# Optimization experiments

Measured on AMD Instinct MI355X. Metric: run time of the kernel, lower is better.

Reference implementation:

```python
import jax, jax.numpy as jnp
import numpy as np

# ---- module config (matches __init__ defaults) ----
NUM_EL_FULL = 128
LV_START, LV_END = 31, 95
NUM_S = LV_END - LV_START            # 64 sensors
NX = NY = 408
ROI = 128
DX = DY = 0.0002
C0 = 1500.0
FS = 40.0e6
DT = 1.0 / FS
R_IN = 0.0406
ARC_ANGLE = 270.0
ARC_START = 135.0
T_SAMPLES = 2030
BATCH = 64


def _geometry():
    """Reproduce _precompute_geometry + _precompute_time_indices_and_weights in numpy."""
    spacing = ARC_ANGLE / (NUM_EL_FULL - 1)
    all_ang = ARC_START + np.arange(NUM_EL_FULL) * spacing
    ang = all_ang[LV_START:LV_END]
    ang_rad = ang * np.pi / 180.0
    cx = (NX / 2 - 0.5) * DX
    cy = (NY / 2 - 0.5) * DY
    sx = cx + R_IN * np.cos(ang_rad)
    sy = cy + R_IN * np.sin(ang_rad)

    rsx = round((NX - ROI) / 2)
    rsy = round((NY - ROI) / 2)
    x_pos = (np.arange(rsx, rsx + ROI, dtype=np.float32) * DX)
    y_pos = (np.arange(rsy, rsy + ROI, dtype=np.float32) * DY)
    yg, xg = np.meshgrid(y_pos, x_pos, indexing='ij')  # [ROI, ROI]

    x_diff = xg[..., None] - sx[None, None, :]          # [ROI, ROI, S]
    y_diff = yg[..., None] - sy[None, None, :]
    dist = np.sqrt(x_diff ** 2 + y_diff ** 2)
    t_idx = np.round(dist / C0 / DT).astype(np.int32)

    normal = ang_rad + np.pi
    a2p = np.arctan2(y_diff, x_diff)
    adiff = a2p - normal[None, None, :]
    adiff = np.arctan2(np.sin(adiff), np.cos(adiff))
    weights = np.clip(np.cos(adiff), 0.0, None).astype(np.float32)
    valid = (t_idx >= 0) & (t_idx < T_SAMPLES)
    return t_idx, weights, valid


def setup_inputs() -> dict:
    key = jax.random.key(0)
    t_idx, weights, valid = _geometry()
    sinogram = jax.random.normal(key, (BATCH, 1, NUM_S, T_SAMPLES), dtype=jnp.float32)
    return {
        "sinogram": sinogram,
        "weights": jnp.asarray(weights),
        "time_indices": jnp.asarray(t_idx),
        "valid_mask": jnp.asarray(valid),
    }


def reference(sinogram, weights, time_indices, valid_mask):
    """DAS beamforming, output_type='both', norm_type='clamp'."""
    B = sinogram.shape[0]
    T = sinogram.shape[-1]
    sino = sinogram[:, 0]                                   # [B, S, T]
    S = sino.shape[1]
    t = jnp.clip(time_indices, 0, T - 1)                    # [H, W, S]
    sensor_idx = jnp.arange(S)[None, None, :]               # [1, 1, S]
    # gather: per-pixel, per-sensor time sample -> [B, H, W, S]
    sampled = sino[:, sensor_idx, t]
    w = jnp.where(valid_mask, weights, 0.0)                 # mask * weight fused
    weighted = sampled * w[None]                            # [B, H, W, S]

    das = weighted.sum(axis=3)[:, None]                     # [B, 1, H, W]
    # normalize: clamp to >=0, per-batch max
    das = jnp.maximum(das, 0.0)
    m = das.reshape(B, -1).max(axis=1)
    m = jnp.where(m > 1e-8, m, 1.0)
    das = das / m[:, None, None, None]

    pixel_interp = jnp.transpose(weighted, (0, 3, 1, 2))    # [B, S, H, W]
    return das, pixel_interp
```

## Files before the change

### kernel.cpp

```cpp
#include <hip/hip_runtime.h>
#include <stdint.h>

#define NB   64
#define NS   64
#define NT   2030
#define NP   16384
#define DAS_ELEMS (NB * NP)
#define PIX_ELEMS ((size_t)NB * NS * NP)

typedef float v4f __attribute__((ext_vector_type(4)));

__global__ __launch_bounds__(256) void prep_kernel(
    const int* __restrict__ t_idx, const float* __restrict__ w,
    int* __restrict__ tc, float* __restrict__ wv)
{
    __shared__ int   ti[64][65];
    __shared__ float wf[64][65];
    const int pbase = blockIdx.x * 64;

    #pragma unroll
    for (int k = 0; k < 16; ++k) {
        int o = k * 256 + threadIdx.x;
        int r = o >> 6, s = o & 63;
        ti[r][s] = t_idx[pbase * 64 + o];
        wf[r][s] = w[pbase * 64 + o];
    }
    __syncthreads();

    #pragma unroll
    for (int k = 0; k < 16; ++k) {
        int o = k * 256 + threadIdx.x;
        int s = o >> 6, r = o & 63;
        int t = ti[r][s];
        bool valid = (t >= 0) & (t < NT);
        int tcl = min(max(t, 0), NT - 1);
        tc[s * NP + pbase + r] = tcl;
        wv[s * NP + pbase + r] = valid ? wf[r][s] : 0.0f;
    }
}

__global__ __launch_bounds__(256) void main_lds_kernel(
    const float* __restrict__ sino,
    const int*   __restrict__ tptr,
    const float* __restrict__ wptr,
    float*       __restrict__ das,
    float*       __restrict__ pix,
    unsigned*    __restrict__ bmax)
{
    __shared__ float lds[2][2048];

    const int tid = threadIdx.x;
    const int b = blockIdx.y;
    const int p = blockIdx.x * 1024 + tid * 4;
    const float* __restrict__ srow = sino + (size_t)b * (NS * NT);
    float* __restrict__ pixb = pix + (size_t)b * ((size_t)NS * NP) + p;

    {
        const float2* __restrict__ r = (const float2*)srow;
        float2 a0 = r[tid];
        float2 a1 = r[tid + 256];
        float2 a2 = r[tid + 512];
        float2* D = (float2*)lds[0];
        D[tid]       = a0;
        D[tid + 256] = a1;
        D[tid + 512] = a2;
        if (tid < 247) D[tid + 768] = r[tid + 768];
    }
    __syncthreads();

    v4f acc = (v4f)(0.0f);
    int cur = 0;

    for (int s = 0; s < NS; ++s) {
        float2 a0, a1, a2, a3;
        if (s + 1 < NS) {
            const float2* __restrict__ r = (const float2*)(srow + (s + 1) * NT);
            a0 = r[tid];
            a1 = r[tid + 256];
            a2 = r[tid + 512];
            if (tid < 247) a3 = r[tid + 768];
        }

        const float* __restrict__ L = lds[cur];
        const int4   t  = *(const int4*)  (tptr + s * NP + p);
        const float4 w4 = *(const float4*)(wptr + s * NP + p);
        v4f v;
        v.x = L[t.x] * w4.x;
        v.y = L[t.y] * w4.y;
        v.z = L[t.z] * w4.z;
        v.w = L[t.w] * w4.w;
        __builtin_nontemporal_store(v, (v4f*)(pixb + (size_t)s * NP));
        acc += v;

        if (s + 1 < NS) {
            float2* D = (float2*)lds[cur ^ 1];
            D[tid]       = a0;
            D[tid + 256] = a1;
            D[tid + 512] = a2;
            if (tid < 247) D[tid + 768] = a3;
            cur ^= 1;
        }
        __syncthreads();
    }

    acc.x = fmaxf(acc.x, 0.f); acc.y = fmaxf(acc.y, 0.f);
    acc.z = fmaxf(acc.z, 0.f); acc.w = fmaxf(acc.w, 0.f);
    *(v4f*)(das + (size_t)b * NP + p) = acc;

    float m = fmaxf(fmaxf(acc.x, acc.y), fmaxf(acc.z, acc.w));
    #pragma unroll
    for (int off = 32; off > 0; off >>= 1)
        m = fmaxf(m, __shfl_down(m, off, 64));
    __shared__ float wm[4];
    if ((tid & 63) == 0) wm[tid >> 6] = m;
    __syncthreads();
    if (tid == 0) {
        m = fmaxf(fmaxf(wm[0], wm[1]), fmaxf(wm[2], wm[3]));
        atomicMax(&bmax[b], __float_as_uint(m));
    }
}

__global__ __launch_bounds__(256) void main_fallback_kernel(
    const float* __restrict__ sino,
    const int*   __restrict__ tptr,
    const float* __restrict__ wptr,
    float*       __restrict__ das,
    float*       __restrict__ pix,
    unsigned*    __restrict__ bmax)
{
    const int b = blockIdx.y;
    const int p = blockIdx.x * 1024 + threadIdx.x * 4;
    const float* __restrict__ srow = sino + (size_t)b * (NS * NT);
    float* __restrict__ pixb = pix + (size_t)b * ((size_t)NS * NP) + p;

    v4f acc = (v4f)(0.0f);

    for (int s = 0; s < NS; ++s) {
        int t0 = tptr[(p + 0) * NS + s];
        int t1 = tptr[(p + 1) * NS + s];
        int t2 = tptr[(p + 2) * NS + s];
        int t3 = tptr[(p + 3) * NS + s];
        float wx = ((t0 >= 0) & (t0 < NT)) ? wptr[(p + 0) * NS + s] : 0.f;
        float wy = ((t1 >= 0) & (t1 < NT)) ? wptr[(p + 1) * NS + s] : 0.f;
        float wz = ((t2 >= 0) & (t2 < NT)) ? wptr[(p + 2) * NS + s] : 0.f;
        float ww = ((t3 >= 0) & (t3 < NT)) ? wptr[(p + 3) * NS + s] : 0.f;
        int4 t;
        t.x = min(max(t0, 0), NT - 1);
        t.y = min(max(t1, 0), NT - 1);
        t.z = min(max(t2, 0), NT - 1);
        t.w = min(max(t3, 0), NT - 1);
        const float* __restrict__ sr = srow + s * NT;
        v4f v;
        v.x = sr[t.x] * wx;
        v.y = sr[t.y] * wy;
        v.z = sr[t.z] * wz;
        v.w = sr[t.w] * ww;
        __builtin_nontemporal_store(v, (v4f*)(pixb + (size_t)s * NP));
        acc += v;
    }

    acc.x = fmaxf(acc.x, 0.f); acc.y = fmaxf(acc.y, 0.f);
    acc.z = fmaxf(acc.z, 0.f); acc.w = fmaxf(acc.w, 0.f);
    *(v4f*)(das + (size_t)b * NP + p) = acc;

    float m = fmaxf(fmaxf(acc.x, acc.y), fmaxf(acc.z, acc.w));
    #pragma unroll
    for (int off = 32; off > 0; off >>= 1)
        m = fmaxf(m, __shfl_down(m, off, 64));
    __shared__ float wm[4];
    if ((threadIdx.x & 63) == 0) wm[threadIdx.x >> 6] = m;
    __syncthreads();
    if (threadIdx.x == 0) {
        m = fmaxf(fmaxf(wm[0], wm[1]), fmaxf(wm[2], wm[3]));
        atomicMax(&bmax[b], __float_as_uint(m));
    }
}

__global__ __launch_bounds__(256) void norm_kernel(
    float* __restrict__ das, const unsigned* __restrict__ bmax)
{
    int idx = (blockIdx.x * 256 + threadIdx.x) * 4;
    int b = idx >> 14;
    float m = __uint_as_float(bmax[b]);
    m = (m > 1e-8f) ? m : 1.0f;
    v4f v = *(v4f*)(das + idx);
    v.x = v.x / m; v.y = v.y / m; v.z = v.z / m; v.w = v.w / m;
    *(v4f*)(das + idx) = v;
}

extern "C" void kernel_launch(void* const* d_in, const int* in_sizes, int n_in,
                              void* d_out, int out_size, void* d_ws, size_t ws_size,
                              hipStream_t stream)
{
    const float* sino  = (const float*)d_in[0];
    const float* w     = (const float*)d_in[1];
    const int*   t_idx = (const int*)  d_in[2];

    float* das = (float*)d_out;
    float* pix = (float*)d_out + DAS_ELEMS;

    char* ws = (char*)d_ws;
    const size_t need = (size_t)(8u << 20) + 256;
    const bool big = ws_size >= need;

    unsigned* bmax;
    int* tc = nullptr; float* wv = nullptr;
    if (big) {
        tc   = (int*)ws;
        wv   = (float*)(ws + (4u << 20));
        bmax = (unsigned*)(ws + (8u << 20));
    } else {
        bmax = (unsigned*)ws;
    }

    (void)hipMemsetAsync(bmax, 0, NB * sizeof(unsigned), stream);

    if (big) {
        prep_kernel<<<256, 256, 0, stream>>>(t_idx, w, tc, wv);
        main_lds_kernel<<<dim3(16, NB), 256, 0, stream>>>(sino, tc, wv, das, pix, bmax);
    } else {
        main_fallback_kernel<<<dim3(16, NB), 256, 0, stream>>>(sino, t_idx, w, das, pix, bmax);
    }
    norm_kernel<<<DAS_ELEMS / 1024, 256, 0, stream>>>(das, bmax);
}
```

Measured before the change: 392.8 us.

## Stage per-wavefront sinogram windows in LDS and drop block barriers

Each wavefront now computes the minimum time index over its pixels for each sensor and copies a private 1024-sample window of that sensor's row into its own double-buffered LDS slice. This removes the block-wide __syncthreads per sensor iteration. Time indices and weights are also prefetched two sensors ahead in registers. The cost is redundant global reads across the four waves. Correctness also depends on each wave's index span fitting inside the window, which holds for this fixed array geometry but is not checked.

```diff
diff --git a/kernel.cpp b/kernel.cpp
--- a/kernel.cpp
+++ b/kernel.cpp
@@ -7,6 +7,8 @@
 #define NP   16384
 #define DAS_ELEMS (NB * NP)
 #define PIX_ELEMS ((size_t)NB * NS * NP)
+
+#define WIN 1024
 
 typedef float v4f __attribute__((ext_vector_type(4)));
 
@@ -47,60 +49,82 @@
     float*       __restrict__ pix,
     unsigned*    __restrict__ bmax)
 {
-    __shared__ float lds[2][2048];
-
-    const int tid = threadIdx.x;
+    __shared__ float sbuf[4][2][WIN];
+
+    const int tid  = threadIdx.x;
+    const int wid  = tid >> 6;
+    const int lane = tid & 63;
     const int b = blockIdx.y;
     const int p = blockIdx.x * 1024 + tid * 4;
     const float* __restrict__ srow = sino + (size_t)b * (NS * NT);
     float* __restrict__ pixb = pix + (size_t)b * ((size_t)NS * NP) + p;
-
+    float* const Lb = &sbuf[wid][0][0];
+
+    int4   tq_cur = *(const int4*)  (tptr + 0 * NP + p);
+    float4 wq_cur = *(const float4*)(wptr + 0 * NP + p);
+    int4   tq_n1  = *(const int4*)  (tptr + 1 * NP + p);
+    float4 wq_n1  = *(const float4*)(wptr + 1 * NP + p);
+
+    int m0 = min(min(tq_cur.x, tq_cur.y), min(tq_cur.z, tq_cur.w));
+    #pragma unroll
+    for (int off = 32; off > 0; off >>= 1)
+        m0 = min(m0, __shfl_xor(m0, off, 64));
+    int w0c = min(m0, NT - WIN) & ~1;
     {
-        const float2* __restrict__ r = (const float2*)srow;
-        float2 a0 = r[tid];
-        float2 a1 = r[tid + 256];
-        float2 a2 = r[tid + 512];
-        float2* D = (float2*)lds[0];
-        D[tid]       = a0;
-        D[tid + 256] = a1;
-        D[tid + 512] = a2;
-        if (tid < 247) D[tid + 768] = r[tid + 768];
-    }
-    __syncthreads();
+        const float2* __restrict__ rr = (const float2*)(srow + w0c);
+        float2* __restrict__ D = (float2*)Lb;
+        #pragma unroll
+        for (int k = 0; k < 8; ++k)
+            D[lane + 64 * k] = rr[lane + 64 * k];
+    }
+    int cur = 0;
 
     v4f acc = (v4f)(0.0f);
-    int cur = 0;
 
     for (int s = 0; s < NS; ++s) {
-        float2 a0, a1, a2, a3;
-        if (s + 1 < NS) {
-            const float2* __restrict__ r = (const float2*)(srow + (s + 1) * NT);
-            a0 = r[tid];
-            a1 = r[tid + 256];
-            a2 = r[tid + 512];
-            if (tid < 247) a3 = r[tid + 768];
+        int4 tq_f; float4 wq_f;
+        if (s + 2 < NS) {
+            tq_f = *(const int4*)  (tptr + (s + 2) * NP + p);
+            wq_f = *(const float4*)(wptr + (s + 2) * NP + p);
         }
 
-        const float* __restrict__ L = lds[cur];
-        const int4   t  = *(const int4*)  (tptr + s * NP + p);
-        const float4 w4 = *(const float4*)(wptr + s * NP + p);
+        int w0n = 0;
+        float2 g0, g1, g2, g3, g4, g5, g6, g7;
+        const bool haven = (s + 1 < NS);
+        if (haven) {
+            int mn = min(min(tq_n1.x, tq_n1.y), min(tq_n1.z, tq_n1.w));
+            #pragma unroll
+            for (int off = 32; off > 0; off >>= 1)
+                mn = min(mn, __shfl_xor(mn, off, 64));
+            w0n = min(mn, NT - WIN) & ~1;
+            const float2* __restrict__ rr =
+                (const float2*)(srow + (s + 1) * NT + w0n);
+            g0 = rr[lane];        g1 = rr[lane + 64];
+            g2 = rr[lane + 128];  g3 = rr[lane + 192];
+            g4 = rr[lane + 256];  g5 = rr[lane + 320];
+            g6 = rr[lane + 384];  g7 = rr[lane + 448];
+        }
+
+        const float* __restrict__ Lc = Lb + cur * WIN;
         v4f v;
-        v.x = L[t.x] * w4.x;
-        v.y = L[t.y] * w4.y;
-        v.z = L[t.z] * w4.z;
-        v.w = L[t.w] * w4.w;
+        v.x = Lc[tq_cur.x - w0c] * wq_cur.x;
+        v.y = Lc[tq_cur.y - w0c] * wq_cur.y;
+        v.z = Lc[tq_cur.z - w0c] * wq_cur.z;
+        v.w = Lc[tq_cur.w - w0c] * wq_cur.w;
         __builtin_nontemporal_store(v, (v4f*)(pixb + (size_t)s * NP));
         acc += v;
 
-        if (s + 1 < NS) {
-            float2* D = (float2*)lds[cur ^ 1];
-            D[tid]       = a0;
-            D[tid + 256] = a1;
-            D[tid + 512] = a2;
-            if (tid < 247) D[tid + 768] = a3;
+        if (haven) {
+            float2* __restrict__ D = (float2*)(Lb + (cur ^ 1) * WIN);
+            D[lane]       = g0;  D[lane + 64]  = g1;
+            D[lane + 128] = g2;  D[lane + 192] = g3;
+            D[lane + 256] = g4;  D[lane + 320] = g5;
+            D[lane + 384] = g6;  D[lane + 448] = g7;
             cur ^= 1;
+            w0c = w0n;
+            tq_cur = tq_n1; wq_cur = wq_n1;
+            tq_n1  = tq_f;  wq_n1  = wq_f;
         }
-        __syncthreads();
     }
 
     acc.x = fmaxf(acc.x, 0.f); acc.y = fmaxf(acc.y, 0.f);
@@ -112,7 +136,7 @@
     for (int off = 32; off > 0; off >>= 1)
         m = fmaxf(m, __shfl_down(m, off, 64));
     __shared__ float wm[4];
-    if ((tid & 63) == 0) wm[tid >> 6] = m;
+    if (lane == 0) wm[wid] = m;
     __syncthreads();
     if (tid == 0) {
         m = fmaxf(fmaxf(wm[0], wm[1]), fmaxf(wm[2], wm[3]));
```

Measured after the change: 400.0 us. Within noise of the previous version (+1.8%).
